# Kernel optimization log

Measured on AMD Instinct MI355X. Metric: run time of the kernel, lower is better.

Reference implementation:

```python
import jax, jax.numpy as jnp
import numpy as np
import math

B, C, L, E, N = 16, 256, 2048, 512, 64
H = 2 * C  # S4 model dimension


def setup_inputs() -> dict:
    key = jax.random.key(0)
    ks = jax.random.split(key, 12)
    inp = {
        "x": jax.random.normal(ks[0], (B, C, L), dtype=jnp.float32),
        "diffusion_emb": jax.random.normal(ks[1], (B, E), dtype=jnp.float32),
        "dp_W": jax.random.normal(ks[2], (C, E), dtype=jnp.float32) / np.sqrt(E).astype(np.float32),
        "dp_b": jnp.zeros((C,), dtype=jnp.float32),
        "in_W": jax.random.normal(ks[3], (H, C), dtype=jnp.float32) / np.sqrt(C).astype(np.float32),
        "in_b": jnp.zeros((H,), dtype=jnp.float32),
        "out_W": jax.random.normal(ks[4], (2 * C, C), dtype=jnp.float32) / np.sqrt(C).astype(np.float32),
        "out_b": jnp.zeros((2 * C,), dtype=jnp.float32),
        "ln1_g": jnp.ones((H,), dtype=jnp.float32),
        "ln1_b": jnp.zeros((H,), dtype=jnp.float32),
        "ln2_g": jnp.ones((H,), dtype=jnp.float32),
        "ln2_b": jnp.zeros((H,), dtype=jnp.float32),
    }
    for i, pre in enumerate(["s41_", "s42_"]):
        k = jax.random.fold_in(key, 100 + i)
        k1, k2, k3, k4, k5 = jax.random.split(k, 5)
        # dt log-uniform in [1e-3, 1e-1] (standard S4 init)
        inp[pre + "log_dt"] = (jax.random.uniform(k1, (H,)) * (math.log(0.1) - math.log(0.001)) + math.log(0.001)).astype(jnp.float32)
        inp[pre + "A_re"] = (-0.5 * jnp.ones((H, N))).astype(jnp.float32)
        inp[pre + "A_im"] = jnp.tile(math.pi * jnp.arange(N, dtype=jnp.float32), (H, 1))
        inp[pre + "C_re"] = jax.random.normal(k2, (H, N), dtype=jnp.float32) * (0.5 ** 0.5)
        inp[pre + "C_im"] = jax.random.normal(k3, (H, N), dtype=jnp.float32) * (0.5 ** 0.5)
        inp[pre + "D"] = jax.random.normal(k4, (H,), dtype=jnp.float32)
        inp[pre + "oW"] = jax.random.normal(k5, (2 * H, H), dtype=jnp.float32) / np.sqrt(H).astype(np.float32)
        inp[pre + "ob"] = jnp.zeros((2 * H,), dtype=jnp.float32)
    return inp


def _s4(u, log_dt, A_re, A_im, C_re, C_im, D, oW, ob):
    # u: [B, H, L]. Diagonal SSM (S4D, ZOH discretization) -> FFT conv -> D skip -> GELU -> GLU output linear.
    Lq = u.shape[-1]
    dt = jnp.exp(log_dt)                       # [H]
    A = A_re + 1j * A_im                       # [H, N] diagonal state matrix
    Cc = C_re + 1j * C_im                      # [H, N]
    dtA = dt[:, None] * A                      # [H, N]
    Ct = Cc * (jnp.exp(dtA) - 1.0) / A         # ZOH-discretized C*B (B = 1)
    lr = jnp.arange(Lq)
    # Vandermonde kernel: K[h, l] = 2 Re sum_n Ct[h, n] exp(dtA[h, n] * l)
    K = 2.0 * jnp.real(jnp.einsum("hn,hnl->hl", Ct, jnp.exp(dtA[:, :, None] * lr)))  # [H, L]
    nfft = 2 * Lq
    y = jnp.fft.irfft(jnp.fft.rfft(u, n=nfft) * jnp.fft.rfft(K, n=nfft), n=nfft)[..., :Lq]
    y = y + D[None, :, None] * u
    y = jax.nn.gelu(y)
    y = jnp.einsum("oh,bhl->bol", oW, y) + ob[None, :, None]  # [B, 2H, L]
    a, b = jnp.split(y, 2, axis=1)             # GLU over channel dim
    return a * jax.nn.sigmoid(b)               # [B, H, L]


def _ln(y, g, b):
    # LayerNorm over the channel dim (module rearranges b c l -> b l c, LN(C), back)
    mu = jnp.mean(y, axis=1, keepdims=True)
    var = jnp.var(y, axis=1, keepdims=True)
    return (y - mu) * jax.lax.rsqrt(var + 1e-5) * g[None, :, None] + b[None, :, None]


def reference(x, diffusion_emb, dp_W, dp_b, in_W, in_b, out_W, out_b,
              ln1_g, ln1_b, ln2_g, ln2_b,
              s41_log_dt, s41_A_re, s41_A_im, s41_C_re, s41_C_im, s41_D, s41_oW, s41_ob,
              s42_log_dt, s42_A_re, s42_A_im, s42_C_re, s42_C_im, s42_D, s42_oW, s42_ob):
    d = diffusion_emb @ dp_W.T + dp_b          # [B, C] -> broadcast as [B, C, 1]
    y = x + d[:, :, None]
    y = jnp.einsum("oc,bcl->bol", in_W, y) + in_b[None, :, None]   # 1x1 conv: [B, 2C, L]
    y = _s4(y, s41_log_dt, s41_A_re, s41_A_im, s41_C_re, s41_C_im, s41_D, s41_oW, s41_ob)
    y = _ln(y, ln1_g, ln1_b)
    y = _s4(y, s42_log_dt, s42_A_re, s42_A_im, s42_C_re, s42_C_im, s42_D, s42_oW, s42_ob)
    y = _ln(y, ln2_g, ln2_b)
    gate, filt = jnp.split(y, 2, axis=1)
    y = jax.nn.sigmoid(gate) * jnp.tanh(filt)  # [B, C, L]
    y = jnp.einsum("oc,bcl->bol", out_W, y) + out_b[None, :, None]  # [B, 2C, L]
    residual, skip = jnp.split(y, 2, axis=1)
    return ((x + residual) / math.sqrt(2.0), skip)
```

## Files before the change

### kernel.cpp

```cpp
#include <hip/hip_runtime.h>
#include <math.h>

#define Bsz 16
#define Cch 256
#define Lsq 2048
#define Emb 512
#define Nst 64
#define Hch 512
#define KGP 2240

typedef _Float16 f16;
typedef _Float16 f16x8 __attribute__((ext_vector_type(8)));
typedef _Float16 f16x4 __attribute__((ext_vector_type(4)));
typedef float f32x4 __attribute__((ext_vector_type(4)));
typedef uint32_t u32x4 __attribute__((ext_vector_type(4)));

__device__ __forceinline__ float sigmoidf_(float x) { return 1.0f/(1.0f + __expf(-x)); }
__device__ __forceinline__ float gelu_tanh(float y) {
  float z = 0.7978845608028654f*(y + 0.044715f*y*y*y);
  return 0.5f*y*(1.0f + tanhf(z));
}

__device__ __forceinline__ void gload_lds16(const f16* g, f16* l) {
  __builtin_amdgcn_global_load_lds(
      (const __attribute__((address_space(1))) void*)g,
      (__attribute__((address_space(3))) void*)l, 16, 0, 0);
}


__global__ void k_emb(const float* __restrict__ emb, const float* __restrict__ dpW,
                      const float* __restrict__ dpb, float* __restrict__ d) {
  int b = blockIdx.x, c = threadIdx.x;
  const float* e = emb + b*Emb;
  const float* w = dpW + c*Emb;
  float s = dpb[c];
  for (int k = 0; k < Emb; ++k) s += e[k]*w[k];
  d[b*Cch + c] = s;
}

__global__ void k_f2h(const float* __restrict__ src, f16* __restrict__ dst, int n) {
  int i = blockIdx.x*256 + threadIdx.x;
  if (i < n) dst[i] = (f16)src[i];
}

__global__ void k_addemb(const float* __restrict__ x, const float* __restrict__ d,
                         f16* __restrict__ xd) {
  int i = blockIdx.x*256 + threadIdx.x;
  const float4* x4 = (const float4*)x;
  float4 v = x4[i];
  int bc = (i*4)/Lsq;
  float dd = d[bc];
  f16x4 o;
  o[0] = (f16)(v.x+dd); o[1] = (f16)(v.y+dd); o[2] = (f16)(v.z+dd); o[3] = (f16)(v.w+dd);
  ((f16x4*)xd)[i] = o;
}

__global__ void k_s4prep(const float* __restrict__ log_dt,
                         const float* __restrict__ A_re, const float* __restrict__ A_im,
                         const float* __restrict__ C_re, const float* __restrict__ C_im,
                         float* __restrict__ w_re, float* __restrict__ w_im,
                         float* __restrict__ ccr, float* __restrict__ cci) {
  int i = blockIdx.x*256 + threadIdx.x;
  if (i >= Hch*Nst) return;
  int h = i >> 6;
  float dt = expf(log_dt[h]);
  float Ar = A_re[i], Ai = A_im[i];
  float er = expf(dt*Ar);
  float wr = er*cosf(dt*Ai), wi = er*sinf(dt*Ai);
  float mag = Ar*Ar + Ai*Ai;
  float nr = wr - 1.0f, ni = wi;
  float qr = (nr*Ar + ni*Ai)/mag, qi = (ni*Ar - nr*Ai)/mag;
  float cr = C_re[i], ci = C_im[i];
  float tr = cr*qr - ci*qi, ti = cr*qi + ci*qr;
  w_re[i] = wr; w_im[i] = wi; ccr[i] = 2.0f*tr; cci[i] = -2.0f*ti;
}

__global__ __launch_bounds__(256) void k_kgen(
    const float* __restrict__ w_re, const float* __restrict__ w_im,
    const float* __restrict__ ccr, const float* __restrict__ cci,
    const float* __restrict__ Dvec,
    f16* __restrict__ Ke, f16* __restrict__ Ko) {
  __shared__ float2 wbt[64][65];
  __shared__ float2 wat[32][66];
  __shared__ float2 ccs[64];
  __shared__ float Kf[2048];
  int h = blockIdx.x, tid = threadIdx.x;
  if (tid < 64) {
    int n = tid;
    double wr = (double)w_re[h*64+n], wi = (double)w_im[h*64+n];
    double br = 1.0, bi = 0.0;
    for (int j = 0; j < 64; ++j) {
      wbt[n][j] = make_float2((float)br, (float)bi);
      double t = br*wr - bi*wi; bi = br*wi + bi*wr; br = t;
    }
    double ar = 1.0, ai = 0.0;
    for (int a = 0; a < 32; ++a) {
      wat[a][n] = make_float2((float)ar, (float)ai);
      double t = ar*br - ai*bi; ai = ar*bi + ai*br; ar = t;
    }
    ccs[n] = make_float2(ccr[h*64+n], cci[h*64+n]);
  }
  __syncthreads();
  int lane = tid & 63, wv = tid >> 6;
  float acc[8] = {0.f,0.f,0.f,0.f,0.f,0.f,0.f,0.f};
  for (int n = 0; n < 64; ++n) {
    float2 wb = wbt[n][lane];
    float2 cc = ccs[n];
    float tr = fmaf(cc.y, wb.y,  cc.x*wb.x);
    float ti = fmaf(cc.y, wb.x, -cc.x*wb.y);
    #pragma unroll
    for (int li = 0; li < 8; ++li) {
      float2 wa = wat[wv + 4*li][n];
      acc[li] = fmaf(wa.x, tr, acc[li]);
      acc[li] = fmaf(wa.y, ti, acc[li]);
    }
  }
  #pragma unroll
  for (int li = 0; li < 8; ++li)
    Kf[(wv + 4*li)*64 + lane] = acc[li];
  __syncthreads();
  if (tid == 0) Kf[0] += Dvec[h];
  __syncthreads();
  f16* keh = Ke + (size_t)h*KGP;
  f16* koh = Ko + (size_t)h*KGP;
  for (int q = tid; q < KGP; q += 256) {
    float e = (q < 2048) ? Kf[2047 - q] : 0.f;
    float o = (q < 2047) ? Kf[2046 - q] : 0.f;
    keh[q] = (f16)e; koh[q] = (f16)o;
  }
}

__device__ __forceinline__ f16x8 ldfrag(const f16* __restrict__ ke,
                                        const f16* __restrict__ ko, int q) {
  const f16* p = (q & 1) ? (ko + (q - 1)) : (ke + q);
  union { uint32_t u[4]; f16x8 v; } r;
  const uint32_t* pu = (const uint32_t*)p;
  r.u[0] = pu[0]; r.u[1] = pu[1]; r.u[2] = pu[2]; r.u[3] = pu[3];
  return r.v;
}

__global__ __launch_bounds__(256) void k_conv(
    const f16* __restrict__ u, const f16* __restrict__ Ke, const f16* __restrict__ Ko,
    f16* __restrict__ g) {
  __shared__ __align__(16) f16 Ul[16*2048];
  int h = blockIdx.x, tid = threadIdx.x;
  {
    int b = tid >> 4, pr = tid & 15;
    const f16* src = u + ((size_t)b*Hch + h)*Lsq;
    f16* dst = &Ul[b*2048];
    #pragma unroll
    for (int c = 0; c < 16; ++c) {
      int gs = c*16 + pr;
      *(f16x8*)&dst[(gs ^ b)*8] = *(const f16x8*)(src + gs*8);
    }
  }
  __syncthreads();
  int wv = tid >> 6, lane = tid & 63;
  int m = lane & 15, qd = lane >> 4;
  const f16* keh = Ke + (size_t)h*KGP;
  const f16* koh = Ko + (size_t)h*KGP;
  f16* gb = g + ((size_t)m*Hch + h)*Lsq;
  const f16* ulb = &Ul[m*2048];
  for (int pass = 0; pass < 4; ++pass) {
    int P = pass*4 + ((wv + pass) & 3);
    int i0 = P*128;
    int qb0 = 2047 - i0 - m + qd*8;
    f32x4 acc[8];
    #pragma unroll
    for (int t = 0; t < 8; ++t) acc[t] = (f32x4){0.f,0.f,0.f,0.f};
    f16x8 W[8];
    #pragma unroll
    for (int t = 0; t < 8; ++t) W[t] = ldfrag(keh, koh, qb0 - 16*t);
    int steps = 4*(P+1);
    for (int s4i = 0; s4i < steps; s4i += 4) {
      #pragma unroll
      for (int ph = 0; ph < 4; ++ph) {
        int s = s4i + ph;
        f16x8 bf = *(const f16x8*)&ulb[((4*s + qd) ^ m)*8];
        f16x8 nf0 = ldfrag(keh, koh, qb0 + 32*(s+1));
        f16x8 nf1 = ldfrag(keh, koh, qb0 - 16 + 32*(s+1));
        #pragma unroll
        for (int t = 0; t < 8; ++t)
          acc[t] = __builtin_amdgcn_mfma_f32_16x16x32_f16(W[(t - 2*ph) & 7], bf, acc[t], 0, 0, 0);
        W[(6 - 2*ph) & 7] = nf0;
        W[(7 - 2*ph) & 7] = nf1;
      }
    }
    #pragma unroll
    for (int t = 0; t < 8; ++t) {
      f16x4 o;
      #pragma unroll
      for (int r = 0; r < 4; ++r) o[r] = (f16)gelu_tanh(acc[t][r]);
      *(f16x4*)&gb[i0 + 16*t + qd*4] = o;
    }
  }
}

template<int KD, int MODE>
__global__ __launch_bounds__(256) void k_gemm(
    const f16* __restrict__ W, const f16* __restrict__ Bact,
    const float* __restrict__ bias, const float* __restrict__ xres,
    float* __restrict__ outF, f16* __restrict__ outH) {
  constexpr int TOFF = (MODE == 1) ? 512 : 256;
  constexpr int NK = KD/32;
  __shared__ __align__(16) f16 As[2][2*128*32];
  __shared__ __align__(16) uint32_t Bs[2][16*132];
  int tid = threadIdx.x;
  int wv = tid >> 6, lane = tid & 63;
  int nt = blockIdx.x;
  int mt = blockIdx.y;
  int bb = nt >> 4;
  int l0 = (nt & 15)*128;
  int m0 = mt*128;
  int wm = (wv & 1)*64, wn = (wv >> 1)*64;
  int qd = lane >> 4, ln16 = lane & 15;

  f32x4 acc[2][4][4];
  #pragma unroll
  for (int t = 0; t < 2; ++t)
    for (int i = 0; i < 4; ++i)
      for (int j = 0; j < 4; ++j)
        acc[t][i][j] = (f32x4){0.f,0.f,0.f,0.f};

  const f16* Bbase = Bact + (size_t)bb*KD*Lsq + l0;
  int q16 = tid >> 4, nch = tid & 15;

  auto stageA = [&](int buf, int kk) {
    #pragma unroll
    for (int i = 0; i < 4; ++i) {
      int gbase = (wv*4 + i)*64;
      int G = gbase + lane;
      int t = G >> 9;
      int row = (G >> 2) & 127;
      int gsw = (G & 3) ^ (row & 3);
      const f16* src = W + (size_t)(m0 + row + t*TOFF)*KD + kk + gsw*8;
      gload_lds16(src, &As[buf][gbase*8]);
    }
  };
  f16x8 rb0, rb1;
  auto loadB = [&](int kk) {
    const f16* b0 = Bbase + (size_t)(kk + 2*q16)*Lsq + nch*8;
    rb0 = *(const f16x8*)b0;
    rb1 = *(const f16x8*)(b0 + Lsq);
  };
  auto packB = [&](int buf) {
    union { uint32_t w[8]; u32x4 v[2]; } pk;
    #pragma unroll
    for (int e = 0; e < 8; ++e) {
      union { f16 h2[2]; uint32_t u; } t2;
      t2.h2[0] = rb0[e]; t2.h2[1] = rb1[e];
      pk.w[e] = t2.u;
    }
    *(u32x4*)&Bs[buf][q16*132 + nch*8]     = pk.v[0];
    *(u32x4*)&Bs[buf][q16*132 + nch*8 + 4] = pk.v[1];
  };
  auto compute = [&](int buf) {
    f16x8 afr[2][4];
    #pragma unroll
    for (int i = 0; i < 4; ++i)
      for (int t = 0; t < 2; ++t) {
        int row = wm + i*16 + ln16;
        int gp = qd ^ (ln16 & 3);
        afr[t][i] = *(const f16x8*)&As[buf][((t*128 + row)*4 + gp)*8];
      }
    f16x8 bfr[4];
    #pragma unroll
    for (int j = 0; j < 4; ++j) {
      union { uint32_t w2[4]; f16x8 v; } bu;
      #pragma unroll
      for (int r2 = 0; r2 < 4; ++r2) bu.w2[r2] = Bs[buf][(qd*4 + r2)*132 + wn + j*16 + ln16];
      bfr[j] = bu.v;
    }
    #pragma unroll
    for (int j = 0; j < 4; ++j)
      for (int i = 0; i < 4; ++i)
        for (int t = 0; t < 2; ++t)
          acc[t][i][j] = __builtin_amdgcn_mfma_f32_16x16x32_f16(afr[t][i], bfr[j], acc[t][i][j], 0, 0, 0);
  };

  stageA(0, 0);
  loadB(0);
  packB(0);
  __syncthreads();

  int cur = 0;
  for (int t = 0; t < NK; ++t) {
    if (t + 1 < NK) {
      stageA(cur ^ 1, (t + 1)*32);
      loadB((t + 1)*32);
    }
    compute(cur);
    if (t + 1 < NK) packB(cur ^ 1);
    __syncthreads();
    cur ^= 1;
  }

  #pragma unroll
  for (int i = 0; i < 4; ++i)
    for (int j = 0; j < 4; ++j)
      for (int r = 0; r < 4; ++r) {
        int ml = wm + i*16 + qd*4 + r;
        int nl = wn + j*16 + ln16;
        int mg = m0 + ml;
        int l  = l0 + nl;
        if (MODE == 0) {
          outH[((size_t)bb*Hch + mg)*Lsq + l]       = (f16)(acc[0][i][j][r] + bias[mg]);
          outH[((size_t)bb*Hch + mg + 256)*Lsq + l] = (f16)(acc[1][i][j][r] + bias[mg + 256]);
        } else if (MODE == 1) {
          float va = acc[0][i][j][r] + bias[mg];
          float vb = acc[1][i][j][r] + bias[512 + mg];
          outH[((size_t)bb*Hch + mg)*Lsq + l] = (f16)(va * sigmoidf_(vb));
        } else {
          size_t idx = ((size_t)bb*Cch + mg)*Lsq + l;
          float v0 = acc[0][i][j][r] + bias[mg];
          outF[idx] = (v0 + xres[idx]) * 0.7071067811865476f;
          float v1 = acc[1][i][j][r] + bias[mg + 256];
          outF[(size_t)Bsz*Cch*Lsq + idx] = v1;
        }
      }
}

template<int MODE>
__global__ __launch_bounds__(256) void k_ln(const f16* __restrict__ v,
                                            const float* __restrict__ gam, const float* __restrict__ bet,
                                            float* __restrict__ outF, f16* __restrict__ outH) {
  __shared__ float red[2][4][64];
  int b = blockIdx.x >> 5;
  int l = (blockIdx.x & 31)*64 + (threadIdx.x & 63);
  int wv = threadIdx.x >> 6, lane = threadIdx.x & 63;
  const f16* base = v + (size_t)b*Hch*Lsq + l;
  float s = 0.f, s2 = 0.f;
  for (int h = wv*128; h < wv*128 + 128; ++h) {
    float xv = (float)base[(size_t)h*Lsq];
    s += xv; s2 += xv*xv;
  }
  red[0][wv][lane] = s; red[1][wv][lane] = s2;
  __syncthreads();
  s  = red[0][0][lane] + red[0][1][lane] + red[0][2][lane] + red[0][3][lane];
  s2 = red[1][0][lane] + red[1][1][lane] + red[1][2][lane] + red[1][3][lane];
  float mu = s*(1.0f/Hch);
  float var = s2*(1.0f/Hch) - mu*mu;
  float rs = rsqrtf(var + 1e-5f);
  if (MODE == 0) {
    f16* ob = outH + (size_t)b*Hch*Lsq + l;
    for (int h = wv*128; h < wv*128 + 128; ++h)
      ob[(size_t)h*Lsq] = (f16)(((float)base[(size_t)h*Lsq] - mu)*rs*gam[h] + bet[h]);
  } else {
    f16* ob = outH + (size_t)b*Cch*Lsq + l;
    for (int c = wv*64; c < wv*64 + 64; ++c) {
      float xg = ((float)base[(size_t)c*Lsq] - mu)*rs*gam[c] + bet[c];
      float xf = ((float)base[(size_t)(c+Cch)*Lsq] - mu)*rs*gam[c+Cch] + bet[c+Cch];
      float xfc = fminf(fmaxf(xf, -15.f), 15.f);
      float e = __expf(2.f*xfc);
      ob[(size_t)c*Lsq] = (f16)(sigmoidf_(xg) * ((e-1.f)/(e+1.f)));
    }
  }
}

extern "C" void kernel_launch(void* const* d_in, const int* in_sizes, int n_in,
                              void* d_out, int out_size, void* d_ws, size_t ws_size,
                              hipStream_t stream) {
  const float* x    = (const float*)d_in[0];
  const float* emb  = (const float*)d_in[1];
  const float* dpW  = (const float*)d_in[2];
  const float* dpb  = (const float*)d_in[3];
  const float* inW  = (const float*)d_in[4];
  const float* inb  = (const float*)d_in[5];
  const float* outW = (const float*)d_in[6];
  const float* outb = (const float*)d_in[7];
  const float* ln1g = (const float*)d_in[8];
  const float* ln1b = (const float*)d_in[9];
  const float* ln2g = (const float*)d_in[10];
  const float* ln2b = (const float*)d_in[11];
  const float* s4[2][8];
  for (int ly = 0; ly < 2; ++ly)
    for (int k = 0; k < 8; ++k) s4[ly][k] = (const float*)d_in[12 + ly*8 + k];

  char* p = (char*)d_ws;
  auto alloc = [&](size_t bytes) { char* r = p; p += (bytes + 255) & ~(size_t)255; return r; };
  f16* inW16  = (f16*)alloc((size_t)Hch*Cch*2);
  f16* oW16_0 = (f16*)alloc((size_t)2*Hch*Hch*2);
  f16* oW16_1 = (f16*)alloc((size_t)2*Hch*Hch*2);
  f16* outW16 = (f16*)alloc((size_t)2*Cch*Cch*2);
  float* dbuf = (float*)alloc((size_t)Bsz*Cch*4);
  float* prm[2][4];
  for (int ly = 0; ly < 2; ++ly)
    for (int k = 0; k < 4; ++k) prm[ly][k] = (float*)alloc((size_t)Hch*Nst*4);
  f16* kge[2], *kgo[2];
  for (int ly = 0; ly < 2; ++ly) {
    kge[ly] = (f16*)alloc((size_t)Hch*KGP*2);
    kgo[ly] = (f16*)alloc((size_t)Hch*KGP*2);
  }
  f16*  xd   = (f16*)alloc((size_t)Bsz*Cch*Lsq*2);
  f16*  u16g = (f16*)alloc((size_t)Bsz*Hch*Lsq*2);
  f16*  gbuf = (f16*)alloc((size_t)Bsz*Hch*Lsq*2);
  f16*  glu  = (f16*)alloc((size_t)Bsz*Hch*Lsq*2);
  f16*  oW16[2] = {oW16_0, oW16_1};

  k_emb<<<Bsz, Cch, 0, stream>>>(emb, dpW, dpb, dbuf);
  k_f2h<<<(Hch*Cch+255)/256, 256, 0, stream>>>(inW, inW16, Hch*Cch);
  k_f2h<<<(2*Hch*Hch+255)/256, 256, 0, stream>>>(s4[0][6], oW16_0, 2*Hch*Hch);
  k_f2h<<<(2*Hch*Hch+255)/256, 256, 0, stream>>>(s4[1][6], oW16_1, 2*Hch*Hch);
  k_f2h<<<(2*Cch*Cch+255)/256, 256, 0, stream>>>(outW, outW16, 2*Cch*Cch);
  for (int ly = 0; ly < 2; ++ly) {
    k_s4prep<<<(Hch*Nst+255)/256, 256, 0, stream>>>(s4[ly][0], s4[ly][1], s4[ly][2],
        s4[ly][3], s4[ly][4], prm[ly][0], prm[ly][1], prm[ly][2], prm[ly][3]);
    k_kgen<<<Hch, 256, 0, stream>>>(prm[ly][0], prm[ly][1], prm[ly][2], prm[ly][3],
        s4[ly][5], kge[ly], kgo[ly]);
  }
  k_addemb<<<(Bsz*Cch*Lsq/4)/256, 256, 0, stream>>>(x, dbuf, xd);

  dim3 gg4(256, 4), gg2(256, 2), bl(256);
  k_gemm<Cch, 0><<<gg2, bl, 0, stream>>>(inW16, xd, inb, nullptr, nullptr, u16g);
  k_conv<<<Hch, 256, 0, stream>>>(u16g, kge[0], kgo[0], gbuf);
  k_gemm<Hch, 1><<<gg4, bl, 0, stream>>>(oW16[0], gbuf, s4[0][7], nullptr, nullptr, glu);
  k_ln<0><<<Bsz*32, 256, 0, stream>>>(glu, ln1g, ln1b, nullptr, u16g);
  k_conv<<<Hch, 256, 0, stream>>>(u16g, kge[1], kgo[1], gbuf);
  k_gemm<Hch, 1><<<gg4, bl, 0, stream>>>(oW16[1], gbuf, s4[1][7], nullptr, nullptr, glu);
  k_ln<1><<<Bsz*32, 256, 0, stream>>>(glu, ln2g, ln2b, nullptr, xd);
  k_gemm<Cch, 2><<<gg2, bl, 0, stream>>>(outW16, xd, outb, x, (float*)d_out, nullptr);
}
```

Before: 533.3 us.

## Deepen GEMM prefetch pipeline, remap blocks XCD-aware, reswizzle A tile LDS

The GEMM main loop now keeps loads two K-steps ahead, using explicit vmcnt/lgkmcnt waits and raw barriers instead of __syncthreads. The grid becomes 1D with a remap that spreads consecutive block IDs across the 8 XCDs, so blocks sharing B tiles co-locate for L2 reuse. The A tile LDS layout changes to an interleaved 8-group XOR swizzle, and MFMA sections get raised wave priority. The hand-tuned waitcnt counts are fragile and could race if the compiler's instruction ordering differs from what they assume.

Result: slower. 591.5 us (+10.9%).

```diff
diff --git a/kernel.cpp b/kernel.cpp
--- a/kernel.cpp
+++ b/kernel.cpp
@@ -26,6 +26,8 @@
       (const __attribute__((address_space(1))) void*)g,
       (__attribute__((address_space(3))) void*)l, 16, 0, 0);
 }
+
+#define SBAR() __builtin_amdgcn_sched_barrier(0)
 
 
 __global__ void k_emb(const float* __restrict__ emb, const float* __restrict__ dpW,
@@ -203,12 +205,17 @@
     float* __restrict__ outF, f16* __restrict__ outH) {
   constexpr int TOFF = (MODE == 1) ? 512 : 256;
   constexpr int NK = KD/32;
-  __shared__ __align__(16) f16 As[2][2*128*32];
+  constexpr int MT = (MODE == 1) ? 4 : 2;
+  __shared__ __align__(16) f16 As[2][128*8*8];
   __shared__ __align__(16) uint32_t Bs[2][16*132];
   int tid = threadIdx.x;
   int wv = tid >> 6, lane = tid & 63;
-  int nt = blockIdx.x;
-  int mt = blockIdx.y;
+
+  int nwg = 256*MT;
+  int bid = blockIdx.x;
+  int lin = (bid & 7)*(nwg >> 3) + (bid >> 3);
+  int mt = lin % MT;
+  int nt = lin / MT;
   int bb = nt >> 4;
   int l0 = (nt & 15)*128;
   int m0 = mt*128;
@@ -230,10 +237,10 @@
     for (int i = 0; i < 4; ++i) {
       int gbase = (wv*4 + i)*64;
       int G = gbase + lane;
-      int t = G >> 9;
-      int row = (G >> 2) & 127;
-      int gsw = (G & 3) ^ (row & 3);
-      const f16* src = W + (size_t)(m0 + row + t*TOFF)*KD + kk + gsw*8;
+      int row = G >> 3;
+      int gsw = (G & 7) ^ (row & 7);
+      int t = gsw >> 2;
+      const f16* src = W + (size_t)(m0 + row + t*TOFF)*KD + kk + (gsw & 3)*8;
       gload_lds16(src, &As[buf][gbase*8]);
     }
   };
@@ -260,8 +267,8 @@
     for (int i = 0; i < 4; ++i)
       for (int t = 0; t < 2; ++t) {
         int row = wm + i*16 + ln16;
-        int gp = qd ^ (ln16 & 3);
-        afr[t][i] = *(const f16x8*)&As[buf][((t*128 + row)*4 + gp)*8];
+        int g = (t*4 + qd) ^ (row & 7);
+        afr[t][i] = *(const f16x8*)&As[buf][(row*8 + g)*8];
       }
     f16x8 bfr[4];
     #pragma unroll
@@ -271,27 +278,47 @@
       for (int r2 = 0; r2 < 4; ++r2) bu.w2[r2] = Bs[buf][(qd*4 + r2)*132 + wn + j*16 + ln16];
       bfr[j] = bu.v;
     }
+    __builtin_amdgcn_s_setprio(1);
     #pragma unroll
     for (int j = 0; j < 4; ++j)
       for (int i = 0; i < 4; ++i)
         for (int t = 0; t < 2; ++t)
           acc[t][i][j] = __builtin_amdgcn_mfma_f32_16x16x32_f16(afr[t][i], bfr[j], acc[t][i][j], 0, 0, 0);
+    __builtin_amdgcn_s_setprio(0);
   };
 
   stageA(0, 0);
   loadB(0);
+  SBAR();
+  asm volatile("s_waitcnt vmcnt(4)" ::: "memory");
+  SBAR();
   packB(0);
-  __syncthreads();
+  stageA(1, 32);
+  loadB(32);
+  SBAR();
+  asm volatile("s_waitcnt vmcnt(6) lgkmcnt(0)" ::: "memory");
+  SBAR();
+  __builtin_amdgcn_s_barrier();
 
   int cur = 0;
   for (int t = 0; t < NK; ++t) {
+    compute(cur);
+    asm volatile("s_waitcnt lgkmcnt(0)" ::: "memory");
+    SBAR();
+    __builtin_amdgcn_s_barrier();
     if (t + 1 < NK) {
-      stageA(cur ^ 1, (t + 1)*32);
-      loadB((t + 1)*32);
-    }
-    compute(cur);
-    if (t + 1 < NK) packB(cur ^ 1);
-    __syncthreads();
+      asm volatile("s_waitcnt vmcnt(0)" ::: "memory");
+      SBAR();
+      packB(cur ^ 1);
+    }
+    if (t + 2 < NK) {
+      stageA(cur, (t + 2)*32);
+      loadB((t + 2)*32);
+    }
+    SBAR();
+    asm volatile("s_waitcnt lgkmcnt(0)" ::: "memory");
+    SBAR();
+    __builtin_amdgcn_s_barrier();
     cur ^= 1;
   }
 
@@ -410,13 +437,13 @@
   }
   k_addemb<<<(Bsz*Cch*Lsq/4)/256, 256, 0, stream>>>(x, dbuf, xd);
 
-  dim3 gg4(256, 4), gg2(256, 2), bl(256);
-  k_gemm<Cch, 0><<<gg2, bl, 0, stream>>>(inW16, xd, inb, nullptr, nullptr, u16g);
+  dim3 bl(256);
+  k_gemm<Cch, 0><<<512, bl, 0, stream>>>(inW16, xd, inb, nullptr, nullptr, u16g);
   k_conv<<<Hch, 256, 0, stream>>>(u16g, kge[0], kgo[0], gbuf);
-  k_gemm<Hch, 1><<<gg4, bl, 0, stream>>>(oW16[0], gbuf, s4[0][7], nullptr, nullptr, glu);
+  k_gemm<Hch, 1><<<1024, bl, 0, stream>>>(oW16[0], gbuf, s4[0][7], nullptr, nullptr, glu);
   k_ln<0><<<Bsz*32, 256, 0, stream>>>(glu, ln1g, ln1b, nullptr, u16g);
   k_conv<<<Hch, 256, 0, stream>>>(u16g, kge[1], kgo[1], gbuf);
-  k_gemm<Hch, 1><<<gg4, bl, 0, stream>>>(oW16[1], gbuf, s4[1][7], nullptr, nullptr, glu);
+  k_gemm<Hch, 1><<<1024, bl, 0, stream>>>(oW16[1], gbuf, s4[1][7], nullptr, nullptr, glu);
   k_ln<1><<<Bsz*32, 256, 0, stream>>>(glu, ln2g, ln2b, nullptr, xd);
-  k_gemm<Cch, 2><<<gg2, bl, 0, stream>>>(outW16, xd, outb, x, (float*)d_out, nullptr);
-}
+  k_gemm<Cch, 2><<<512, bl, 0, stream>>>(outW16, xd, outb, x, (float*)d_out, nullptr);
+}
```

## Widen GEMM tile to 128x256 with 512 threads, XCD-aware block remap

Applied to the files above, without the earlier changes.

The k_gemm kernel moves from 256-thread blocks with 128x128 tiles to 512-thread blocks covering 256 columns of L, so each A tile is reused across twice as many columns. The LDS layout for A becomes an 8-group XOR swizzle interleaving both GLU halves per row, and the B tile stride widens to match. Grid launch becomes 1D with a remap that spreads consecutive block IDs across the 8 XCDs, and s_setprio is raised around the MFMA block to favour matrix issue. The aim is less redundant A traffic and better L2 locality, at the cost of fewer, larger workgroups and more LDS per block. The epilogue (not shown) may still assume the old tile indexing.

After: 514.2 us. 1.04x faster.

```diff
diff --git a/kernel.cpp b/kernel.cpp
--- a/kernel.cpp
+++ b/kernel.cpp
@@ -197,20 +197,25 @@
 }
 
 template<int KD, int MODE>
-__global__ __launch_bounds__(256) void k_gemm(
+__global__ __launch_bounds__(512) void k_gemm(
     const f16* __restrict__ W, const f16* __restrict__ Bact,
     const float* __restrict__ bias, const float* __restrict__ xres,
     float* __restrict__ outF, f16* __restrict__ outH) {
   constexpr int TOFF = (MODE == 1) ? 512 : 256;
   constexpr int NK = KD/32;
-  __shared__ __align__(16) f16 As[2][2*128*32];
-  __shared__ __align__(16) uint32_t Bs[2][16*132];
+  constexpr int MT = (MODE == 1) ? 4 : 2;
+  __shared__ __align__(16) f16 As[2][128*8*8];
+  __shared__ __align__(16) uint32_t Bs[2][16*260];
   int tid = threadIdx.x;
   int wv = tid >> 6, lane = tid & 63;
-  int nt = blockIdx.x;
-  int mt = blockIdx.y;
-  int bb = nt >> 4;
-  int l0 = (nt & 15)*128;
+
+  int nwg = 128*MT;
+  int bid = blockIdx.x;
+  int lin = (bid & 7)*(nwg >> 3) + (bid >> 3);
+  int mt = lin % MT;
+  int nt = lin / MT;
+  int bb = nt >> 3;
+  int l0 = (nt & 7)*256;
   int m0 = mt*128;
   int wm = (wv & 1)*64, wn = (wv >> 1)*64;
   int qd = lane >> 4, ln16 = lane & 15;
@@ -223,17 +228,17 @@
         acc[t][i][j] = (f32x4){0.f,0.f,0.f,0.f};
 
   const f16* Bbase = Bact + (size_t)bb*KD*Lsq + l0;
-  int q16 = tid >> 4, nch = tid & 15;
+  int q16 = tid >> 5, nch = tid & 31;
 
   auto stageA = [&](int buf, int kk) {
     #pragma unroll
-    for (int i = 0; i < 4; ++i) {
-      int gbase = (wv*4 + i)*64;
+    for (int i = 0; i < 2; ++i) {
+      int gbase = (wv*2 + i)*64;
       int G = gbase + lane;
-      int t = G >> 9;
-      int row = (G >> 2) & 127;
-      int gsw = (G & 3) ^ (row & 3);
-      const f16* src = W + (size_t)(m0 + row + t*TOFF)*KD + kk + gsw*8;
+      int row = G >> 3;
+      int gsw = (G & 7) ^ (row & 7);
+      int t = gsw >> 2;
+      const f16* src = W + (size_t)(m0 + row + t*TOFF)*KD + kk + (gsw & 3)*8;
       gload_lds16(src, &As[buf][gbase*8]);
     }
   };
@@ -251,8 +256,8 @@
       t2.h2[0] = rb0[e]; t2.h2[1] = rb1[e];
       pk.w[e] = t2.u;
     }
-    *(u32x4*)&Bs[buf][q16*132 + nch*8]     = pk.v[0];
-    *(u32x4*)&Bs[buf][q16*132 + nch*8 + 4] = pk.v[1];
+    *(u32x4*)&Bs[buf][q16*260 + nch*8]     = pk.v[0];
+    *(u32x4*)&Bs[buf][q16*260 + nch*8 + 4] = pk.v[1];
   };
   auto compute = [&](int buf) {
     f16x8 afr[2][4];
@@ -260,22 +265,24 @@
     for (int i = 0; i < 4; ++i)
       for (int t = 0; t < 2; ++t) {
         int row = wm + i*16 + ln16;
-        int gp = qd ^ (ln16 & 3);
-        afr[t][i] = *(const f16x8*)&As[buf][((t*128 + row)*4 + gp)*8];
+        int g = (t*4 + qd) ^ (row & 7);
+        afr[t][i] = *(const f16x8*)&As[buf][(row*8 + g)*8];
       }
     f16x8 bfr[4];
     #pragma unroll
     for (int j = 0; j < 4; ++j) {
       union { uint32_t w2[4]; f16x8 v; } bu;
       #pragma unroll
-      for (int r2 = 0; r2 < 4; ++r2) bu.w2[r2] = Bs[buf][(qd*4 + r2)*132 + wn + j*16 + ln16];
+      for (int r2 = 0; r2 < 4; ++r2) bu.w2[r2] = Bs[buf][(qd*4 + r2)*260 + wn + j*16 + ln16];
       bfr[j] = bu.v;
     }
+    __builtin_amdgcn_s_setprio(1);
     #pragma unroll
     for (int j = 0; j < 4; ++j)
       for (int i = 0; i < 4; ++i)
         for (int t = 0; t < 2; ++t)
           acc[t][i][j] = __builtin_amdgcn_mfma_f32_16x16x32_f16(afr[t][i], bfr[j], acc[t][i][j], 0, 0, 0);
+    __builtin_amdgcn_s_setprio(0);
   };
 
   stageA(0, 0);
@@ -410,13 +417,13 @@
   }
   k_addemb<<<(Bsz*Cch*Lsq/4)/256, 256, 0, stream>>>(x, dbuf, xd);
 
-  dim3 gg4(256, 4), gg2(256, 2), bl(256);
-  k_gemm<Cch, 0><<<gg2, bl, 0, stream>>>(inW16, xd, inb, nullptr, nullptr, u16g);
+  dim3 bl(512);
+  k_gemm<Cch, 0><<<256, bl, 0, stream>>>(inW16, xd, inb, nullptr, nullptr, u16g);
   k_conv<<<Hch, 256, 0, stream>>>(u16g, kge[0], kgo[0], gbuf);
-  k_gemm<Hch, 1><<<gg4, bl, 0, stream>>>(oW16[0], gbuf, s4[0][7], nullptr, nullptr, glu);
+  k_gemm<Hch, 1><<<512, bl, 0, stream>>>(oW16[0], gbuf, s4[0][7], nullptr, nullptr, glu);
   k_ln<0><<<Bsz*32, 256, 0, stream>>>(glu, ln1g, ln1b, nullptr, u16g);
   k_conv<<<Hch, 256, 0, stream>>>(u16g, kge[1], kgo[1], gbuf);
-  k_gemm<Hch, 1><<<gg4, bl, 0, stream>>>(oW16[1], gbuf, s4[1][7], nullptr, nullptr, glu);
+  k_gemm<Hch, 1><<<512, bl, 0, stream>>>(oW16[1], gbuf, s4[1][7], nullptr, nullptr, glu);
   k_ln<1><<<Bsz*32, 256, 0, stream>>>(glu, ln2g, ln2b, nullptr, xd);
-  k_gemm<Cch, 2><<<gg2, bl, 0, stream>>>(outW16, xd, outb, x, (float*)d_out, nullptr);
-}
+  k_gemm<Cch, 2><<<256, bl, 0, stream>>>(outW16, xd, outb, x, (float*)d_out, nullptr);
+}
```
